# Performance work log

Measured on AMD Instinct MI355X. Metric: run time of the kernel, lower is better.

The kernel has to match this reference:

```python
import jax, jax.numpy as jnp
import numpy as np

CATE_BIN = (512, 128, 256, 256, 64, 256, 256, 16, 256)
NUM_BIN = (64, 16, 128, 64, 128, 64, 512, 512)
TABLE_SIZES = CATE_BIN + NUM_BIN  # 17 tables
EMB_DIM = 16
MAX_ROWS = max(TABLE_SIZES)  # 512; tables padded/stacked for a fused gather
HIDDEN = [256, 256, 128]
OUT = 1
BATCH = 262144
BN_EPS = 1e-5


def setup_inputs() -> dict:
    key = jax.random.key(0)
    ks = jax.random.split(key, 32)
    # indices: per-column cardinality
    cols = [jax.random.randint(jax.random.fold_in(ks[0], i), (BATCH,), 0, n, dtype=jnp.int32)
            for i, n in enumerate(TABLE_SIZES)]
    x = jnp.stack(cols, axis=1)  # [B, 17] int32
    # fused/padded embedding tables: [17, MAX_ROWS, EMB_DIM]
    tables = jax.random.normal(ks[1], (len(TABLE_SIZES), MAX_ROWS, EMB_DIM), dtype=jnp.float32) * 0.05
    d_in = len(TABLE_SIZES) * EMB_DIM  # 272
    dims = [d_in] + HIDDEN
    params = {}
    for i in range(len(HIDDEN)):
        params[f"W{i}"] = jax.random.normal(ks[2 + 4 * i], (dims[i], dims[i + 1]), dtype=jnp.float32) * (1.0 / np.sqrt(dims[i]))
        params[f"b{i}"] = jnp.zeros((dims[i + 1],), dtype=jnp.float32)
        params[f"g{i}"] = jnp.ones((dims[i + 1],), dtype=jnp.float32)
        params[f"be{i}"] = jnp.zeros((dims[i + 1],), dtype=jnp.float32)
    params["Wout"] = jax.random.normal(ks[30], (HIDDEN[-1], OUT), dtype=jnp.float32) * (1.0 / np.sqrt(HIDDEN[-1]))
    params["bout"] = jnp.zeros((OUT,), dtype=jnp.float32)
    return {"x": x, "tables": tables, **params}


def _batchnorm(h, g, b):
    mu = jnp.mean(h, axis=0)
    var = jnp.var(h, axis=0)  # biased, matching torch BN forward
    return g * (h - mu) * jax.lax.rsqrt(var + BN_EPS) + b


def reference(x, tables, W0, b0, g0, be0, W1, b1, g1, be1, W2, b2, g2, be2, Wout, bout):
    # fused table-batched gather: [B, 17, 16] -> [B, 272]
    emb = tables[jnp.arange(tables.shape[0]), x]  # [B, 17, E]
    h = emb.reshape(emb.shape[0], -1)
    for W, b, g, be in ((W0, b0, g0, be0), (W1, b1, g1, be1), (W2, b2, g2, be2)):
        h = jax.nn.relu(h @ W + b)
        h = _batchnorm(h, g, be)
    return h @ Wout + bout
```

## Files before the change

kernel.cpp:

```cpp
#include <hip/hip_runtime.h>
#include <stdint.h>

#define BR 262144
#define NTAB 17
#define MAXR 512
#define DIN 272
#define AS0 296
#define ASM 264
#define NCOPY 32
#define BNEPS 1e-5f

typedef __attribute__((ext_vector_type(8))) short short8;
typedef __attribute__((ext_vector_type(4))) float f32x4;
typedef __attribute__((ext_vector_type(4))) unsigned short ushort4w;

__device__ __forceinline__ unsigned short f2bf(float f) {
  union { float f; unsigned u; } v; v.f = f;
  return (unsigned short)((v.u + 0x7FFFu + ((v.u >> 16) & 1u)) >> 16);
}
__device__ __forceinline__ float bf2f(unsigned short h) {
  union { unsigned u; float f; } v; v.u = ((unsigned)h) << 16;
  return v.f;
}

__global__ void k_prep0(const float* __restrict__ W0, unsigned short* __restrict__ pW0,
                        float* __restrict__ stats) {
  int tid = blockIdx.x * blockDim.x + threadIdx.x;
  int nth = gridDim.x * blockDim.x;
  for (int i = tid; i < NCOPY * 1280; i += nth) stats[i] = 0.f;
  for (int e = tid; e < 9 * 16 * 64; e += nth) {
    int l = e & 63, f = e >> 6;
    int nf = f & 15, ks = f >> 4;
    int col = nf * 16 + (l & 15);
    int kb = ks * 32 + ((l >> 4) << 3);
    unsigned short tmp[8];
#pragma unroll
    for (int j = 0; j < 8; j++) {
      int k = kb + j;
      tmp[j] = f2bf(k < DIN ? W0[k * 256 + col] : 0.f);
    }
    *(short8*)&pW0[(size_t)e * 8] = *(short8*)tmp;
  }
}

template <int KP, int NP>
__global__ void k_fold(const float* __restrict__ stats, int offSum, int offSq,
                       const float* __restrict__ g, const float* __restrict__ be,
                       const float* __restrict__ W, const float* __restrict__ b,
                       unsigned short* __restrict__ pW, float* __restrict__ bOut) {
  __shared__ float sa[KP], sc[KP];
  int tid = threadIdx.x;
  if (tid < KP) {
    float s = 0.f, q = 0.f;
    for (int c = 0; c < NCOPY; c++) {
      s += stats[c * 1280 + offSum + tid];
      q += stats[c * 1280 + offSq + tid];
    }
    float mu = s * (1.f / BR);
    float var = fmaxf(q * (1.f / BR) - mu * mu, 0.f);
    float a = g[tid] * rsqrtf(var + BNEPS);
    sa[tid] = a;
    sc[tid] = be[tid] - mu * a;
  }
  __syncthreads();
  const int NFT = NP / 16;
  const int ENT = (KP / 32) * NFT * 64;
  for (int e = blockIdx.x * blockDim.x + tid; e < ENT; e += gridDim.x * blockDim.x) {
    int l = e & 63, f = e >> 6;
    int nf = f % NFT, ks = f / NFT;
    int col = nf * 16 + (l & 15);
    int kb = ks * 32 + ((l >> 4) << 3);
    unsigned short tmp[8];
#pragma unroll
    for (int j = 0; j < 8; j++) {
      int k = kb + j;
      tmp[j] = f2bf(sa[k] * W[k * NP + col]);
    }
    *(short8*)&pW[(size_t)e * 8] = *(short8*)tmp;
  }
  if (blockIdx.x == 0 && tid < NP) {
    float s = b[tid];
    for (int k = 0; k < KP; k++) s += sc[k] * W[k * NP + tid];
    bOut[tid] = s;
  }
}

__global__ void k_foldout(const float* __restrict__ stats, int offSum, int offSq,
                          const float* __restrict__ g, const float* __restrict__ be,
                          const float* __restrict__ Wout, const float* __restrict__ bout,
                          float* __restrict__ woutp, float* __restrict__ boutp) {
  __shared__ float red[128];
  int tid = threadIdx.x;
  float s = 0.f, q = 0.f;
  for (int c = 0; c < NCOPY; c++) {
    s += stats[c * 1280 + offSum + tid];
    q += stats[c * 1280 + offSq + tid];
  }
  float mu = s * (1.f / BR);
  float var = fmaxf(q * (1.f / BR) - mu * mu, 0.f);
  float a = g[tid] * rsqrtf(var + BNEPS);
  float c = be[tid] - mu * a;
  float w = Wout[tid];
  woutp[tid] = a * w;
  red[tid] = c * w;
  __syncthreads();
  for (int st = 64; st > 0; st >>= 1) {
    if (tid < st) red[tid] += red[tid + st];
    __syncthreads();
  }
  if (tid == 0) boutp[0] = red[0] + bout[0];
}

template <int KSTEPS, int N, int AST, int MF>
__device__ __forceinline__ void gemm_body(unsigned short* As, const unsigned short* __restrict__ pW,
                                          const float* __restrict__ bias, unsigned short* __restrict__ Y,
                                          int brow, float* ssum, float* ssq,
                                          float* __restrict__ gsum, float* __restrict__ gsq) {
  const int tid = threadIdx.x;
  const int lane = tid & 63, wave = tid >> 6;
  constexpr int WC = N / 64;
  const int wc = wave % WC, wr = wave / WC;
  const int wrow = wr * (MF * 16);
  const int wcolf = wc * 4;
  const int arow = lane & 15;
  const int koff = (lane >> 4) << 3;
  const int grp = lane >> 4;

  f32x4 zero4 = {0.f, 0.f, 0.f, 0.f};
  f32x4 acc[MF][4];
#pragma unroll
  for (int mf = 0; mf < MF; mf++)
#pragma unroll
    for (int nf = 0; nf < 4; nf++) acc[mf][nf] = zero4;

  short8 bcur[4], bnxt[4];
#pragma unroll
  for (int nf = 0; nf < 4; nf++)
    bcur[nf] = *(const short8*)&pW[(size_t)((wcolf + nf) * 64 + lane) * 8];

#pragma unroll
  for (int ks = 0; ks < KSTEPS; ks++) {
    if (ks + 1 < KSTEPS) {
#pragma unroll
      for (int nf = 0; nf < 4; nf++)
        bnxt[nf] = *(const short8*)&pW[(size_t)(((ks + 1) * (N / 16) + wcolf + nf) * 64 + lane) * 8];
    }
#pragma unroll
    for (int mf = 0; mf < MF; mf++) {
      short8 am = *(const short8*)&As[(wrow + mf * 16 + arow) * AST + ks * 32 + koff];
#pragma unroll
      for (int nf = 0; nf < 4; nf++)
        acc[mf][nf] = __builtin_amdgcn_mfma_f32_16x16x32_bf16(bcur[nf], am, acc[mf][nf], 0, 0, 0);
    }
#pragma unroll
    for (int nf = 0; nf < 4; nf++) bcur[nf] = bnxt[nf];
  }

  __syncthreads();

#pragma unroll
  for (int nf = 0; nf < 4; nf++) {
    const int c0 = (wcolf + nf) * 16 + grp * 4;
    f32x4 bb = *(const f32x4*)&bias[c0];
    float s[4] = {0.f, 0.f, 0.f, 0.f}, q[4] = {0.f, 0.f, 0.f, 0.f};
#pragma unroll
    for (int mf = 0; mf < MF; mf++) {
      const int r = wrow + mf * 16 + arow;
      unsigned short o[4];
#pragma unroll
      for (int j = 0; j < 4; j++) {
        float v = fmaxf(acc[mf][nf][j] + bb[j], 0.f);
        o[j] = f2bf(v);
        s[j] += v;
        q[j] += v * v;
      }
      *(ushort4w*)&As[r * AST + c0] = *(ushort4w*)o;
    }
#pragma unroll
    for (int d = 1; d < 16; d <<= 1) {
#pragma unroll
      for (int j = 0; j < 4; j++) {
        s[j] += __shfl_xor(s[j], d, 64);
        q[j] += __shfl_xor(q[j], d, 64);
      }
    }
    if ((lane & 15) == 0) {
#pragma unroll
      for (int j = 0; j < 4; j++) {
        atomicAdd(&ssum[c0 + j], s[j]);
        atomicAdd(&ssq[c0 + j], q[j]);
      }
    }
  }
  __syncthreads();

  constexpr int CH = N / 8;
  for (int i = tid; i < 64 * CH; i += 256) {
    int row = i / CH, ch = i % CH;
    *(short8*)&Y[(size_t)(brow + row) * 256 + ch * 8] = *(const short8*)&As[row * AST + ch * 8];
  }
  if (tid < N) {
    atomicAdd(&gsum[tid], ssum[tid]);
    atomicAdd(&gsq[tid], ssq[tid]);
  }
}

__global__ __launch_bounds__(256, 4) void k_gemm0(const int* __restrict__ x, const float* __restrict__ tables,
                        const unsigned short* __restrict__ pW, const float* __restrict__ bias,
                        unsigned short* __restrict__ Y, float* __restrict__ stats, int offSum, int offSq) {
  __shared__ unsigned short As[64 * AS0];
  __shared__ float ssum[256], ssq[256];
  const int tid = threadIdx.x;
  if (tid < 256) { ssum[tid] = 0.f; ssq[tid] = 0.f; }
  const int brow = blockIdx.x * 64;
  for (int t = tid; t < 64 * NTAB; t += 256) {
    int row = t / NTAB;
    int tbl = t - row * NTAB;
    int idx = x[brow * NTAB + t];
    const float* src = tables + ((size_t)tbl * MAXR + idx) * 16;
    f32x4 v0 = ((const f32x4*)src)[0];
    f32x4 v1 = ((const f32x4*)src)[1];
    f32x4 v2 = ((const f32x4*)src)[2];
    f32x4 v3 = ((const f32x4*)src)[3];
    unsigned short tmp[16];
#pragma unroll
    for (int j = 0; j < 4; j++) {
      tmp[j] = f2bf(v0[j]);
      tmp[4 + j] = f2bf(v1[j]);
      tmp[8 + j] = f2bf(v2[j]);
      tmp[12 + j] = f2bf(v3[j]);
    }
    unsigned base = row * AS0 + tbl * 16;
    *(short8*)&As[base] = *(short8*)&tmp[0];
    *(short8*)&As[base + 8] = *(short8*)&tmp[8];
  }
  short8 z8 = {0, 0, 0, 0, 0, 0, 0, 0};
  for (int t = tid; t < 64; t += 256) {
    *(short8*)&As[t * AS0 + 272] = z8;
    *(short8*)&As[t * AS0 + 280] = z8;
    *(short8*)&As[t * AS0 + 288] = z8;
  }
  __syncthreads();
  float* gsum = stats + (size_t)(blockIdx.x & (NCOPY - 1)) * 1280 + offSum;
  float* gsq  = stats + (size_t)(blockIdx.x & (NCOPY - 1)) * 1280 + offSq;
  gemm_body<9, 256, AS0, 4>(As, pW, bias, Y, brow, ssum, ssq, gsum, gsq);
}

template <int N, int MF>
__global__ __launch_bounds__(256, 4) void k_gemm_mid(const unsigned short* __restrict__ Yin,
                           const unsigned short* __restrict__ pW, const float* __restrict__ bias,
                           unsigned short* __restrict__ Y, float* __restrict__ stats, int offSum, int offSq) {
  __shared__ unsigned short As[64 * ASM];
  __shared__ float ssum[256], ssq[256];
  const int tid = threadIdx.x;
  if (tid < 256) { ssum[tid] = 0.f; ssq[tid] = 0.f; }
  const int brow = blockIdx.x * 64;
  for (int i = tid; i < 64 * 32; i += 256) {
    int row = i >> 5, c16 = i & 31;
    short8 v = *(const short8*)&Yin[((size_t)(brow + row)) * 256 + c16 * 8];
    *(short8*)&As[row * ASM + c16 * 8] = v;
  }
  __syncthreads();
  float* gsum = stats + (size_t)(blockIdx.x & (NCOPY - 1)) * 1280 + offSum;
  float* gsq  = stats + (size_t)(blockIdx.x & (NCOPY - 1)) * 1280 + offSq;
  gemm_body<8, N, ASM, MF>(As, pW, bias, Y, brow, ssum, ssq, gsum, gsq);
}

__global__ void k_out(const unsigned short* __restrict__ Y, const float* __restrict__ woutp,
                      const float* __restrict__ boutp, float* __restrict__ out) {
  __shared__ float w[128];
  const int tid = threadIdx.x;
  if (tid < 128) w[tid] = woutp[tid];
  __syncthreads();
  const int lane = tid & 63, wave = tid >> 6;
  const int sub = lane & 7, rloc = lane >> 3;
  const int row = blockIdx.x * 32 + wave * 8 + rloc;
  const unsigned short* yr = &Y[(size_t)row * 256 + sub * 16];
  short8 v0 = *(const short8*)yr;
  short8 v1 = *(const short8*)(yr + 8);
  float acc = 0.f;
#pragma unroll
  for (int j = 0; j < 8; j++) acc += bf2f((unsigned short)v0[j]) * w[sub * 16 + j];
#pragma unroll
  for (int j = 0; j < 8; j++) acc += bf2f((unsigned short)v1[j]) * w[sub * 16 + 8 + j];
  acc += __shfl_xor(acc, 1, 64);
  acc += __shfl_xor(acc, 2, 64);
  acc += __shfl_xor(acc, 4, 64);
  if (sub == 0) out[row] = acc + boutp[0];
}

extern "C" void kernel_launch(void* const* d_in, const int* in_sizes, int n_in,
                              void* d_out, int out_size, void* d_ws, size_t ws_size,
                              hipStream_t stream) {
  const int* x = (const int*)d_in[0];
  const float* tables = (const float*)d_in[1];
  const float* W0 = (const float*)d_in[2];
  const float* b0 = (const float*)d_in[3];
  const float* g0 = (const float*)d_in[4];
  const float* be0 = (const float*)d_in[5];
  const float* W1 = (const float*)d_in[6];
  const float* b1 = (const float*)d_in[7];
  const float* g1 = (const float*)d_in[8];
  const float* be1 = (const float*)d_in[9];
  const float* W2 = (const float*)d_in[10];
  const float* b2 = (const float*)d_in[11];
  const float* g2 = (const float*)d_in[12];
  const float* be2 = (const float*)d_in[13];
  const float* Wout = (const float*)d_in[14];
  const float* bout = (const float*)d_in[15];
  float* out = (float*)d_out;

  char* ws = (char*)d_ws;
  unsigned short* Y = (unsigned short*)ws;
  size_t off = (size_t)BR * 256 * 2;
  unsigned short* pW0 = (unsigned short*)(ws + off); off += (size_t)9 * 16 * 64 * 8 * 2;
  unsigned short* pW1 = (unsigned short*)(ws + off); off += (size_t)8 * 16 * 64 * 8 * 2;
  unsigned short* pW2 = (unsigned short*)(ws + off); off += (size_t)8 * 8 * 64 * 8 * 2;
  float* b1p = (float*)(ws + off); off += 1024;
  float* b2p = (float*)(ws + off); off += 512;
  float* woutp = (float*)(ws + off); off += 512;
  float* boutp = (float*)(ws + off); off += 256;
  float* stats = (float*)(ws + off); off += (size_t)NCOPY * 1280 * 4;

  const int oS0 = 0, oQ0 = 256, oS1 = 512, oQ1 = 768, oS2 = 1024, oQ2 = 1152;

  k_prep0<<<64, 256, 0, stream>>>(W0, pW0, stats);
  k_gemm0<<<BR / 64, 256, 0, stream>>>(x, tables, pW0, b0, Y, stats, oS0, oQ0);
  k_fold<256, 256><<<16, 256, 0, stream>>>(stats, oS0, oQ0, g0, be0, W1, b1, pW1, b1p);
  k_gemm_mid<256, 4><<<BR / 64, 256, 0, stream>>>(Y, pW1, b1p, Y, stats, oS1, oQ1);
  k_fold<256, 128><<<16, 256, 0, stream>>>(stats, oS1, oQ1, g1, be1, W2, b2, pW2, b2p);
  k_gemm_mid<128, 2><<<BR / 64, 256, 0, stream>>>(Y, pW2, b2p, Y, stats, oS2, oQ2);
  k_foldout<<<1, 128, 0, stream>>>(stats, oS2, oQ2, g2, be2, Wout, bout, woutp, boutp);
  k_out<<<BR / 32, 256, 0, stream>>>(Y, woutp, boutp, out);
}
```

Before: 258.8 us.

## Pre-convert embedding tables to bf16 and stage indices in shared memory

The fp32 embedding tables are converted to bf16 once inside the prep kernel. The first GEMM kernel now gathers 16-byte bf16 halves directly instead of reading 64-byte fp32 rows and converting them per block. Indices are first loaded coalesced into shared memory, and the gather is split into two phases with an extra barrier. Launch bounds are also relaxed from 4 to 3 blocks per CU for both GEMM kernels, which allows more registers but may reduce occupancy.

```diff
diff --git a/kernel.cpp b/kernel.cpp
--- a/kernel.cpp
+++ b/kernel.cpp
@@ -23,11 +23,21 @@
   return v.f;
 }
 
-__global__ void k_prep0(const float* __restrict__ W0, unsigned short* __restrict__ pW0,
+__global__ void k_prep0(const float* __restrict__ W0, const float* __restrict__ tables,
+                        unsigned short* __restrict__ pW0, unsigned short* __restrict__ tb,
                         float* __restrict__ stats) {
   int tid = blockIdx.x * blockDim.x + threadIdx.x;
   int nth = gridDim.x * blockDim.x;
   for (int i = tid; i < NCOPY * 1280; i += nth) stats[i] = 0.f;
+  for (int e = tid; e < 17408; e += nth) {
+    const float* src = tables + (size_t)e * 8;
+    f32x4 v0 = ((const f32x4*)src)[0];
+    f32x4 v1 = ((const f32x4*)src)[1];
+    unsigned short tmp[8];
+#pragma unroll
+    for (int j = 0; j < 4; j++) { tmp[j] = f2bf(v0[j]); tmp[4 + j] = f2bf(v1[j]); }
+    *(short8*)&tb[(size_t)e * 8] = *(short8*)tmp;
+  }
   for (int e = tid; e < 9 * 16 * 64; e += nth) {
     int l = e & 63, f = e >> 6;
     int nf = f & 15, ks = f >> 4;
@@ -205,35 +215,16 @@
   }
 }
 
-__global__ __launch_bounds__(256, 4) void k_gemm0(const int* __restrict__ x, const float* __restrict__ tables,
+__global__ __launch_bounds__(256, 3) void k_gemm0(const int* __restrict__ x, const unsigned short* __restrict__ tb,
                         const unsigned short* __restrict__ pW, const float* __restrict__ bias,
                         unsigned short* __restrict__ Y, float* __restrict__ stats, int offSum, int offSq) {
   __shared__ unsigned short As[64 * AS0];
+  __shared__ int sx[64 * NTAB];
   __shared__ float ssum[256], ssq[256];
   const int tid = threadIdx.x;
   if (tid < 256) { ssum[tid] = 0.f; ssq[tid] = 0.f; }
   const int brow = blockIdx.x * 64;
-  for (int t = tid; t < 64 * NTAB; t += 256) {
-    int row = t / NTAB;
-    int tbl = t - row * NTAB;
-    int idx = x[brow * NTAB + t];
-    const float* src = tables + ((size_t)tbl * MAXR + idx) * 16;
-    f32x4 v0 = ((const f32x4*)src)[0];
-    f32x4 v1 = ((const f32x4*)src)[1];
-    f32x4 v2 = ((const f32x4*)src)[2];
-    f32x4 v3 = ((const f32x4*)src)[3];
-    unsigned short tmp[16];
-#pragma unroll
-    for (int j = 0; j < 4; j++) {
-      tmp[j] = f2bf(v0[j]);
-      tmp[4 + j] = f2bf(v1[j]);
-      tmp[8 + j] = f2bf(v2[j]);
-      tmp[12 + j] = f2bf(v3[j]);
-    }
-    unsigned base = row * AS0 + tbl * 16;
-    *(short8*)&As[base] = *(short8*)&tmp[0];
-    *(short8*)&As[base + 8] = *(short8*)&tmp[8];
-  }
+  for (int t = tid; t < 64 * NTAB; t += 256) sx[t] = x[brow * NTAB + t];
   short8 z8 = {0, 0, 0, 0, 0, 0, 0, 0};
   for (int t = tid; t < 64; t += 256) {
     *(short8*)&As[t * AS0 + 272] = z8;
@@ -241,13 +232,22 @@
     *(short8*)&As[t * AS0 + 288] = z8;
   }
   __syncthreads();
+  for (int i = tid; i < 64 * NTAB * 2; i += 256) {
+    int r = i / (NTAB * 2);
+    int rem = i - r * (NTAB * 2);
+    int tbl = rem >> 1, half = rem & 1;
+    int idx = sx[r * NTAB + tbl];
+    short8 v = *(const short8*)&tb[((size_t)(tbl * MAXR + idx)) * 16 + half * 8];
+    *(short8*)&As[r * AS0 + tbl * 16 + half * 8] = v;
+  }
+  __syncthreads();
   float* gsum = stats + (size_t)(blockIdx.x & (NCOPY - 1)) * 1280 + offSum;
   float* gsq  = stats + (size_t)(blockIdx.x & (NCOPY - 1)) * 1280 + offSq;
   gemm_body<9, 256, AS0, 4>(As, pW, bias, Y, brow, ssum, ssq, gsum, gsq);
 }
 
 template <int N, int MF>
-__global__ __launch_bounds__(256, 4) void k_gemm_mid(const unsigned short* __restrict__ Yin,
+__global__ __launch_bounds__(256, 3) void k_gemm_mid(const unsigned short* __restrict__ Yin,
                            const unsigned short* __restrict__ pW, const float* __restrict__ bias,
                            unsigned short* __restrict__ Y, float* __restrict__ stats, int offSum, int offSq) {
   __shared__ unsigned short As[64 * ASM];
@@ -321,11 +321,12 @@
   float* woutp = (float*)(ws + off); off += 512;
   float* boutp = (float*)(ws + off); off += 256;
   float* stats = (float*)(ws + off); off += (size_t)NCOPY * 1280 * 4;
+  unsigned short* tb = (unsigned short*)(ws + off); off += (size_t)17 * MAXR * 16 * 2;
 
   const int oS0 = 0, oQ0 = 256, oS1 = 512, oQ1 = 768, oS2 = 1024, oQ2 = 1152;
 
-  k_prep0<<<64, 256, 0, stream>>>(W0, pW0, stats);
-  k_gemm0<<<BR / 64, 256, 0, stream>>>(x, tables, pW0, b0, Y, stats, oS0, oQ0);
+  k_prep0<<<64, 256, 0, stream>>>(W0, tables, pW0, tb, stats);
+  k_gemm0<<<BR / 64, 256, 0, stream>>>(x, tb, pW0, b0, Y, stats, oS0, oQ0);
   k_fold<256, 256><<<16, 256, 0, stream>>>(stats, oS0, oQ0, g0, be0, W1, b1, pW1, b1p);
   k_gemm_mid<256, 4><<<BR / 64, 256, 0, stream>>>(Y, pW1, b1p, Y, stats, oS1, oQ1);
   k_fold<256, 128><<<16, 256, 0, stream>>>(stats, oS1, oQ1, g1, be1, W2, b2, pW2, b2p);
```

New measurement: 251.1 us. -3.0%, faster.
